# Kernel tuning notes

Hardware: AMD Instinct MI355X
Metric: run time of the kernel (lower is better)

Reference implementation:

```python
import jax, jax.numpy as jnp
import numpy as np

N_NODES = 50000
N_EDGES = 800000
D = 128
N_LAYERS = 4


def _sage_conv(x, edge_index, Wl, bl, Wr):
    # PyG SAGEConv (mean aggr): out = lin_l(mean_{j in N(i)} x_j) + lin_r(x_i)
    src, dst = edge_index[0], edge_index[1]
    msgs = x[src]                                            # [E, D] gather
    summed = jax.ops.segment_sum(msgs, dst, num_segments=N_NODES)   # [N, D]
    cnt = jax.ops.segment_sum(jnp.ones((msgs.shape[0],), x.dtype), dst,
                              num_segments=N_NODES)
    mean = summed / jnp.maximum(cnt, 1.0)[:, None]           # [N, D]
    return mean @ Wl.T + bl + x @ Wr.T


def setup_inputs() -> dict:
    key = jax.random.key(0)
    ks = jax.random.split(key, 2 + 3 * N_LAYERS)
    x = jax.random.normal(ks[0], (N_NODES, D), dtype=jnp.float32)
    edge_index = jax.random.randint(ks[1], (2, N_EDGES), 0, N_NODES, dtype=jnp.int64)
    inp = {"x": x, "edge_index": edge_index}
    s = 1.0 / np.sqrt(D)
    for i in range(N_LAYERS):
        inp[f"Wl{i}"] = jax.random.uniform(ks[2 + 3 * i], (D, D), jnp.float32, -s, s)
        inp[f"bl{i}"] = jax.random.uniform(ks[3 + 3 * i], (D,), jnp.float32, -s, s)
        inp[f"Wr{i}"] = jax.random.uniform(ks[4 + 3 * i], (D, D), jnp.float32, -s, s)
    return inp


def reference(x, edge_index, Wl0, bl0, Wr0, Wl1, bl1, Wr1, Wl2, bl2, Wr2, Wl3, bl3, Wr3):
    # ReLU only after the first conv, per the original forward.
    h = jax.nn.relu(_sage_conv(x, edge_index, Wl0, bl0, Wr0))
    h = _sage_conv(h, edge_index, Wl1, bl1, Wr1)
    h = _sage_conv(h, edge_index, Wl2, bl2, Wr2)
    h = _sage_conv(h, edge_index, Wl3, bl3, Wr3)
    return h
```

## Files before the change

kernel.cpp:

```cpp
#include <hip/hip_runtime.h>
#include <stdint.h>

#define NN 50000
#define NE 800000
#define NB 196
#define CAST_B 6250
#define CVTW_B 512
#define CNT_B 3125
#define NX 8

typedef short short8 __attribute__((ext_vector_type(8)));
typedef float f32x4 __attribute__((ext_vector_type(4)));
typedef unsigned int uint;
typedef unsigned short ushort;

__device__ __forceinline__ uint rne_bf16(float f) {
    uint x = __float_as_uint(f);
    return (x + 0x7FFFu + ((x >> 16) & 1u)) >> 16;
}
__device__ __forceinline__ float bf_lo(uint d) { return __uint_as_float(d << 16); }
__device__ __forceinline__ float bf_hi(uint d) { return __uint_as_float(d & 0xFFFF0000u); }

__device__ __forceinline__ int ei_is64(const int* __restrict__ ei) {
    return (ei[1] | ei[3] | ei[5] | ei[7]) == 0;
}

__device__ __forceinline__ int xcc_id() {
    int x;
    asm volatile("s_getreg_b32 %0, hwreg(HW_REG_XCC_ID, 0, 32)" : "=s"(x));
    return x & (NX - 1);
}

struct Ptrs8 { const float* p[8]; };

__global__ __launch_bounds__(256) void k_prep(
    const float* __restrict__ x, ushort* __restrict__ xbf, Ptrs8 ps,
    ushort* __restrict__ wbf, const int* __restrict__ ei,
    int* __restrict__ hist, uint* __restrict__ rank) {
    int b = blockIdx.x;
    if (b < CAST_B) {
        int i = b * 256 + threadIdx.x;
        float4 v = ((const float4*)x)[i];
        uint2 o;
        o.x = rne_bf16(v.x) | (rne_bf16(v.y) << 16);
        o.y = rne_bf16(v.z) | (rne_bf16(v.w) << 16);
        ((uint2*)xbf)[i] = o;
    } else if (b < CAST_B + CVTW_B) {
        int idx = (b - CAST_B) * 256 + threadIdx.x;
        int m = idx >> 14;
        int off = idx & 16383;
        wbf[idx] = (ushort)rne_bf16(ps.p[m][off]);
    } else {
        int e = (b - CAST_B - CVTW_B) * 256 + threadIdx.x;
        int is64 = ei_is64(ei);
        int d = is64 ? ei[2 * NE + 2 * e] : ei[NE + e];
        int cid = xcc_id();
        int rk = __hip_atomic_fetch_add(&hist[cid * NN + d], 1,
                                        __ATOMIC_RELAXED,
                                        __HIP_MEMORY_SCOPE_WORKGROUP);
        rank[e] = (uint)rk | ((uint)cid << 16);
    }
}

__global__ __launch_bounds__(256) void k_blocksum(int* __restrict__ hist,
                                                  int* __restrict__ deg,
                                                  int* __restrict__ bsum) {
    __shared__ int s[256];
    int i = blockIdx.x * 256 + threadIdx.x;
    int sum = 0;
    if (i < NN) {
        int run = 0;
#pragma unroll
        for (int c = 0; c < NX; c++) {
            int t = hist[c * NN + i];
            hist[c * NN + i] = run;
            run += t;
        }
        deg[i] = run;
        sum = run;
    }
    s[threadIdx.x] = sum;
    __syncthreads();
    for (int off = 128; off > 0; off >>= 1) {
        if (threadIdx.x < off) s[threadIdx.x] += s[threadIdx.x + off];
        __syncthreads();
    }
    if (threadIdx.x == 0) bsum[blockIdx.x] = s[0];
}

__global__ __launch_bounds__(256) void k_scanb(const int* __restrict__ bsum,
                                               int* __restrict__ boff) {
    __shared__ int s[256];
    int t = threadIdx.x;
    s[t] = (t < NB) ? bsum[t] : 0;
    __syncthreads();
    for (int off = 1; off < 256; off <<= 1) {
        int v = s[t];
        int a = (t >= off) ? s[t - off] : 0;
        __syncthreads();
        s[t] = v + a;
        __syncthreads();
    }
    if (t < NB) boff[t] = (t == 0) ? 0 : s[t - 1];
}

__global__ __launch_bounds__(256) void k_writeptr(const int* __restrict__ deg,
                                                  const int* __restrict__ boff,
                                                  const int* __restrict__ hist,
                                                  int* __restrict__ row_ptr,
                                                  int* __restrict__ rowb,
                                                  float* __restrict__ rinv) {
    __shared__ int s[256];
    int b = blockIdx.x, t = threadIdx.x;
    int i = b * 256 + t;
    int d = (i < NN) ? deg[i] : 0;
    s[t] = d;
    __syncthreads();
    for (int off = 1; off < 256; off <<= 1) {
        int v = s[t];
        int a = (t >= off) ? s[t - off] : 0;
        __syncthreads();
        s[t] = v + a;
        __syncthreads();
    }
    if (i < NN) {
        int pos = boff[b] + s[t] - d;
        row_ptr[i] = pos;
        rinv[i] = 1.0f / (float)max(d, 1);
#pragma unroll
        for (int c = 0; c < NX; c++) rowb[c * NN + i] = pos + hist[c * NN + i];
    }
    if (b == 0 && t == 0) row_ptr[NN] = NE;
}

__global__ void k_fill(const int* __restrict__ ei,
                       const int* __restrict__ rowb,
                       const uint* __restrict__ rank, ushort* __restrict__ col) {
    int e = blockIdx.x * 256 + threadIdx.x;
    if (e >= NE) return;
    int is64 = ei_is64(ei);
    int sv = is64 ? ei[2 * e] : ei[e];
    int dv = is64 ? ei[2 * NE + 2 * e] : ei[NE + e];
    uint r = rank[e];
    int p = rowb[(int)(r >> 16) * NN + dv] + (int)(r & 0xFFFFu);
    col[p] = (ushort)sv;
}

__global__ __launch_bounds__(256) void k_agg3(const ushort* __restrict__ h,
                                              const int* __restrict__ row_ptr,
                                              const ushort* __restrict__ col,
                                              const float* __restrict__ rinv,
                                              ushort* __restrict__ mean) {
    int node = blockIdx.x * 4 + (threadIdx.x >> 6);
    if (node >= NN) return;
    int lane = threadIdx.x & 63;
    int beg = row_ptr[node], end = row_ptr[node + 1];
    const uint* hp = (const uint*)h;
    float a0 = 0.f, a1 = 0.f;
    for (int b = beg; b < end; b += 64) {
        int n = min(64, end - b);
        int c = (int)col[b + min(lane, n - 1)];
        for (int j0 = 0; j0 < n; j0 += 8) {
#pragma unroll
            for (int j = 0; j < 8; j++) {
                int jj = j0 + j;
                int s = __shfl(c, min(jj, n - 1));
                uint v = hp[s * 64 + lane];
                float m = (jj < n) ? 1.f : 0.f;
                a0 = fmaf(m, bf_lo(v), a0);
                a1 = fmaf(m, bf_hi(v), a1);
            }
        }
    }
    float r = rinv[node];
    ((uint*)mean)[node * 64 + lane] = rne_bf16(a0 * r) | (rne_bf16(a1 * r) << 16);
}

__global__ __launch_bounds__(256) void k_gemm_mfma(
    const ushort* __restrict__ Am, const ushort* __restrict__ Ah,
    const ushort* __restrict__ Wlb, const ushort* __restrict__ Wrb,
    const float* __restrict__ bias, float* __restrict__ outf,
    ushort* __restrict__ outb, int relu) {
    const int lane = threadIdx.x & 63;
    const int wave = threadIdx.x >> 6;
    const int l15 = lane & 15;
    const int quad = lane >> 4;
    const int m0 = blockIdx.x * 64 + wave * 16;

    f32x4 acc[8];
#pragma unroll
    for (int t = 0; t < 8; t++) acc[t] = (f32x4){0.f, 0.f, 0.f, 0.f};

    int arow = min(m0 + l15, NN - 1);
    const ushort* Arm = Am + (size_t)arow * 128 + quad * 8;
    const ushort* Arh = Ah + (size_t)arow * 128 + quad * 8;
    const int wro = quad * 8;

#pragma unroll
    for (int half = 0; half < 2; half++) {
        const ushort* Ar = half ? Arh : Arm;
        const ushort* W = half ? Wrb : Wlb;
#pragma unroll
        for (int k0 = 0; k0 < 128; k0 += 32) {
            short8 a = *(const short8*)(Ar + k0);
#pragma unroll
            for (int t = 0; t < 8; t++) {
                short8 b = *(const short8*)(W + (size_t)(t * 16 + l15) * 128 + k0 + wro);
                acc[t] = __builtin_amdgcn_mfma_f32_16x16x32_bf16(a, b, acc[t], 0, 0, 0);
            }
        }
    }

    float bb[8];
#pragma unroll
    for (int t = 0; t < 8; t++) bb[t] = bias[t * 16 + l15];

#pragma unroll
    for (int r = 0; r < 4; r++) {
        int row = m0 + quad * 4 + r;
        if (row < NN) {
#pragma unroll
            for (int t = 0; t < 8; t++) {
                float v = acc[t][r] + bb[t];
                if (relu) v = fmaxf(v, 0.f);
                if (outb) outb[(size_t)row * 128 + t * 16 + l15] = (ushort)rne_bf16(v);
                else outf[(size_t)row * 128 + t * 16 + l15] = v;
            }
        }
    }
}

extern "C" void kernel_launch(void* const* d_in, const int* in_sizes, int n_in,
                              void* d_out, int out_size, void* d_ws, size_t ws_size,
                              hipStream_t stream) {
    const float* x = (const float*)d_in[0];
    const int* ei = (const int*)d_in[1];
    const float* Wl[4] = {(const float*)d_in[2], (const float*)d_in[5],
                          (const float*)d_in[8], (const float*)d_in[11]};
    const float* bl[4] = {(const float*)d_in[3], (const float*)d_in[6],
                          (const float*)d_in[9], (const float*)d_in[12]};
    const float* Wr[4] = {(const float*)d_in[4], (const float*)d_in[7],
                          (const float*)d_in[10], (const float*)d_in[13]};
    float* out = (float*)d_out;

    char* p = (char*)d_ws;
    auto take = [&](size_t bytes) -> char* {
        char* r = p;
        p += (bytes + 255) & ~(size_t)255;
        return r;
    };
    int* hist = (int*)take((size_t)NX * NN * 4);
    int* deg = (int*)take(NN * 4);
    int* row_ptr = (int*)take((NN + 1) * 4);
    int* rowb = (int*)take((size_t)NX * NN * 4);
    float* rinv = (float*)take(NN * 4);
    int* bsum = (int*)take(NB * 4);
    int* boff = (int*)take(NB * 4);
    uint* rank = (uint*)take((size_t)NE * 4);
    ushort* col = (ushort*)take((size_t)NE * 2 + 256);
    ushort* xbf = (ushort*)take((size_t)NN * 128 * 2);
    ushort* h1 = (ushort*)take((size_t)NN * 128 * 2);
    ushort* h2 = (ushort*)take((size_t)NN * 128 * 2);
    ushort* meanbf = (ushort*)take((size_t)NN * 128 * 2);
    ushort* wbf = (ushort*)take(8 * 16384 * 2);

    Ptrs8 ps;
    ps.p[0] = Wl[0]; ps.p[1] = Wr[0]; ps.p[2] = Wl[1]; ps.p[3] = Wr[1];
    ps.p[4] = Wl[2]; ps.p[5] = Wr[2]; ps.p[6] = Wl[3]; ps.p[7] = Wr[3];

    hipMemsetAsync(hist, 0, (size_t)NX * NN * 4, stream);
    k_prep<<<CAST_B + CVTW_B + CNT_B, 256, 0, stream>>>(x, xbf, ps, wbf, ei,
                                                        hist, rank);
    k_blocksum<<<NB, 256, 0, stream>>>(hist, deg, bsum);
    k_scanb<<<1, 256, 0, stream>>>(bsum, boff);
    k_writeptr<<<NB, 256, 0, stream>>>(deg, boff, hist, row_ptr, rowb, rinv);
    k_fill<<<CNT_B, 256, 0, stream>>>(ei, rowb, rank, col);

    const ushort* h = xbf;
    ushort* houts[4] = {h1, h2, h1, nullptr};
    for (int l = 0; l < 4; l++) {
        k_agg3<<<(NN + 3) / 4, 256, 0, stream>>>(h, row_ptr, col, rinv, meanbf);
        k_gemm_mfma<<<(NN + 63) / 64, 256, 0, stream>>>(
            meanbf, h, wbf + (size_t)(2 * l) * 16384,
            wbf + (size_t)(2 * l + 1) * 16384, bl[l], out, houts[l],
            l == 0 ? 1 : 0);
        h = houts[l];
    }
}
```

Measured before the change: 418.7 us.

## Split bf16 features into four column slabs and aggregate per slab

Node features and mean buffers are stored as four 32-column slabs (each node's slice is 64 bytes), and the aggregation kernel runs one block per (slab, 4 nodes). Within a wave, four groups of 16 lanes each gather a different neighbor, and the partial sums are reduced with cross-lane shuffles. The aim is to shrink each slab's working set so gathers hit cache more often and to raise concurrency across neighbors. The cost is four times as many blocks, each re-reading the row pointers and column indices, plus shuffle reductions; the GEMM's load and store addressing is adjusted to the slab layout.

```diff
diff --git a/kernel.cpp b/kernel.cpp
--- a/kernel.cpp
+++ b/kernel.cpp
@@ -8,11 +8,15 @@
 #define CVTW_B 512
 #define CNT_B 3125
 #define NX 8
+#define NCH 4
 
 typedef short short8 __attribute__((ext_vector_type(8)));
 typedef float f32x4 __attribute__((ext_vector_type(4)));
 typedef unsigned int uint;
 typedef unsigned short ushort;
+
+#define SLAB_U (NN * 16)
+#define SLAB_S (NN * 32)
 
 __device__ __forceinline__ uint rne_bf16(float f) {
     uint x = __float_as_uint(f);
@@ -44,7 +48,10 @@
         uint2 o;
         o.x = rne_bf16(v.x) | (rne_bf16(v.y) << 16);
         o.y = rne_bf16(v.z) | (rne_bf16(v.w) << 16);
-        ((uint2*)xbf)[i] = o;
+        int node = i >> 5;
+        int chunk = (i >> 3) & 3;
+        int w = i & 7;
+        ((uint2*)xbf)[((size_t)chunk * NN + node) * 8 + w] = o;
     } else if (b < CAST_B + CVTW_B) {
         int idx = (b - CAST_B) * 256 + threadIdx.x;
         int m = idx >> 14;
@@ -146,34 +153,40 @@
     col[p] = (ushort)sv;
 }
 
-__global__ __launch_bounds__(256) void k_agg3(const ushort* __restrict__ h,
+__global__ __launch_bounds__(256) void k_agg4(const ushort* __restrict__ h,
                                               const int* __restrict__ row_ptr,
                                               const ushort* __restrict__ col,
                                               const float* __restrict__ rinv,
                                               ushort* __restrict__ mean) {
-    int node = blockIdx.x * 4 + (threadIdx.x >> 6);
-    if (node >= NN) return;
+    int chunk = blockIdx.x & 3;
+    int node = (blockIdx.x >> 2) * 4 + (threadIdx.x >> 6);
     int lane = threadIdx.x & 63;
+    int slot = lane >> 4;
+    int d = lane & 15;
     int beg = row_ptr[node], end = row_ptr[node + 1];
-    const uint* hp = (const uint*)h;
+    const uint* hp = (const uint*)h + (size_t)chunk * SLAB_U;
     float a0 = 0.f, a1 = 0.f;
     for (int b = beg; b < end; b += 64) {
         int n = min(64, end - b);
-        int c = (int)col[b + min(lane, n - 1)];
-        for (int j0 = 0; j0 < n; j0 += 8) {
-#pragma unroll
-            for (int j = 0; j < 8; j++) {
-                int jj = j0 + j;
-                int s = __shfl(c, min(jj, n - 1));
-                uint v = hp[s * 64 + lane];
-                float m = (jj < n) ? 1.f : 0.f;
-                a0 = fmaf(m, bf_lo(v), a0);
-                a1 = fmaf(m, bf_hi(v), a1);
-            }
+        int cl = (int)__builtin_nontemporal_load(&col[b + min(lane, n - 1)]);
+#pragma unroll 4
+        for (int j0 = 0; j0 < n; j0 += 4) {
+            int idx = j0 + slot;
+            int s = __shfl(cl, min(idx, n - 1));
+            uint v = hp[s * 16 + d];
+            float m = (idx < n) ? 1.f : 0.f;
+            a0 = fmaf(m, bf_lo(v), a0);
+            a1 = fmaf(m, bf_hi(v), a1);
         }
     }
-    float r = rinv[node];
-    ((uint*)mean)[node * 64 + lane] = rne_bf16(a0 * r) | (rne_bf16(a1 * r) << 16);
+    a0 += __shfl_xor(a0, 16); a0 += __shfl_xor(a0, 32);
+    a1 += __shfl_xor(a1, 16); a1 += __shfl_xor(a1, 32);
+    if (lane < 16) {
+        float r = rinv[node];
+        uint pk = rne_bf16(a0 * r) | (rne_bf16(a1 * r) << 16);
+        __builtin_nontemporal_store(
+            pk, (uint*)mean + ((size_t)chunk * NN + node) * 16 + lane);
+    }
 }
 
 __global__ __launch_bounds__(256) void k_gemm_mfma(
@@ -192,8 +205,8 @@
     for (int t = 0; t < 8; t++) acc[t] = (f32x4){0.f, 0.f, 0.f, 0.f};
 
     int arow = min(m0 + l15, NN - 1);
-    const ushort* Arm = Am + (size_t)arow * 128 + quad * 8;
-    const ushort* Arh = Ah + (size_t)arow * 128 + quad * 8;
+    const ushort* Arm = Am + (size_t)arow * 32 + quad * 8;
+    const ushort* Arh = Ah + (size_t)arow * 32 + quad * 8;
     const int wro = quad * 8;
 
 #pragma unroll
@@ -202,7 +215,7 @@
         const ushort* W = half ? Wrb : Wlb;
 #pragma unroll
         for (int k0 = 0; k0 < 128; k0 += 32) {
-            short8 a = *(const short8*)(Ar + k0);
+            short8 a = *(const short8*)(Ar + (size_t)(k0 >> 5) * SLAB_S);
 #pragma unroll
             for (int t = 0; t < 8; t++) {
                 short8 b = *(const short8*)(W + (size_t)(t * 16 + l15) * 128 + k0 + wro);
@@ -223,8 +236,12 @@
             for (int t = 0; t < 8; t++) {
                 float v = acc[t][r] + bb[t];
                 if (relu) v = fmaxf(v, 0.f);
-                if (outb) outb[(size_t)row * 128 + t * 16 + l15] = (ushort)rne_bf16(v);
-                else outf[(size_t)row * 128 + t * 16 + l15] = v;
+                if (outb) {
+                    outb[((size_t)(t >> 1) * NN + row) * 32 + (t & 1) * 16 + l15] =
+                        (ushort)rne_bf16(v);
+                } else {
+                    outf[(size_t)row * 128 + t * 16 + l15] = v;
+                }
             }
         }
     }
@@ -279,7 +296,7 @@
     const ushort* h = xbf;
     ushort* houts[4] = {h1, h2, h1, nullptr};
     for (int l = 0; l < 4; l++) {
-        k_agg3<<<(NN + 3) / 4, 256, 0, stream>>>(h, row_ptr, col, rinv, meanbf);
+        k_agg4<<<(NN / 4) * NCH, 256, 0, stream>>>(h, row_ptr, col, rinv, meanbf);
         k_gemm_mfma<<<(NN + 63) / 64, 256, 0, stream>>>(
             meanbf, h, wbf + (size_t)(2 * l) * 16384,
             wbf + (size_t)(2 * l + 1) * 16384, bl[l], out, houts[l],
```

Measured after the change: 624.9 us. +49.2%, slower.
